# Kernel optimization log

Hardware: AMD Instinct MI355X
Metric: run time of the kernel (lower is better)

The kernel has to match this reference:

```python
import jax, jax.numpy as jnp
import numpy as np

B, T, H, A = 64, 512, 1024, 256  # T == max_sen_len by construction of attention_u
PAD_VAL = -2.0 ** 22


def setup_inputs() -> dict:
    key = jax.random.key(0)
    k1, k2, k3, k4 = jax.random.split(key, 4)
    inputs = jax.random.normal(k1, (B, T, H), dtype=jnp.float32)
    sen_len = jax.random.randint(k2, (B,), 1, T + 1, dtype=jnp.int32)
    W = jax.random.normal(k3, (H, A), dtype=jnp.float32) * (1.0 / np.sqrt(H))
    b = jnp.zeros((A,), dtype=jnp.float32)
    U = jax.random.normal(k4, (A, T), dtype=jnp.float32) * (1.0 / np.sqrt(A))
    return {"inputs": inputs, "sen_len": sen_len, "W": W, "b": b, "U": U}


def reference(inputs, sen_len, W, b, U):
    # Dense with tanh: [B,T,H] @ [H,A] -> [B,T,A]
    alpha = jnp.tanh(jnp.einsum('bth,ha->bta', inputs, W) + b)
    # Score against attention_u: [B,T,A] @ [A,T] -> [B,T,T]
    scores = jnp.einsum('bta,as->bts', alpha, U)
    # sequence mask over last (key) dim, broadcast over query dim
    mask = jnp.arange(T)[None, :] < sen_len[:, None]        # [B,T]
    scores = jnp.where(mask[:, None, :], scores, jnp.float32(PAD_VAL))
    p = jax.nn.softmax(scores, axis=-1)                     # [B,T,T]
    # Weighted sum pooling: [B,T,T] @ [B,T,H] -> [B,T,H]
    Z = jnp.einsum('bts,bsh->bth', p, inputs)
    # dropout: is_training=False -> identity
    return Z
```

## Files before the change

kernel.cpp:

```cpp
#include <hip/hip_runtime.h>
#include <hip/hip_bf16.h>

typedef short short8 __attribute__((ext_vector_type(8)));
typedef short short4v __attribute__((ext_vector_type(4)));
typedef float f32x4 __attribute__((ext_vector_type(4)));
typedef __bf16 bf16x8 __attribute__((ext_vector_type(8)));

template <int ROWS>
__device__ __forceinline__ void stage2(const __hip_bfloat16* __restrict__ g,
                                       int ld, short* lds, int t) {
    const int w = t >> 6;
    const int lane = t & 63;
#pragma unroll
    for (int i = 0; i < ROWS / 64; ++i) {
        const int cb = i * 512 + w * 64;
        const int c = cb + lane;
        const int row = c >> 3;
        const int kc = (c & 7) ^ (row & 7);
        __builtin_amdgcn_global_load_lds((const void*)(g + (long)row * ld + kc * 8),
                                         (void*)(lds + cb * 8), 16, 0, 0);
    }
}

__global__ __launch_bounds__(512, 2) void gemm_xw_kernel(
    const float* __restrict__ Xf,
    const __hip_bfloat16* __restrict__ Wt,
    __hip_bfloat16* __restrict__ alpha,
    const float* __restrict__ bias) {
    __shared__ __align__(16) short sm[2][24576];

    int bx = blockIdx.x, by = blockIdx.y;
    {
        const int nx = gridDim.x, ny = gridDim.y;
        const int nwg = nx * ny;
        const int lin = bx + nx * by;
        const int swz = (lin & 7) * (nwg >> 3) + (lin >> 3);
        bx = swz % nx;
        by = swz / nx;
    }

    const int t = threadIdx.x;
    const int w = t >> 6, lane = t & 63;
    const int wm = w >> 1, wn = w & 1;
    const int fr = lane & 15, quad = lane >> 4;

    const float* Ab = Xf + (long)by * 256 * 1024;
    const __hip_bfloat16* Bb = Wt + (long)bx * 128 * 1024;

    int arow[4], akc[4];
#pragma unroll
    for (int i = 0; i < 4; ++i) {
        const int c = i * 512 + t;
        arow[i] = c >> 3;
        akc[i] = ((c & 7) ^ (arow[i] & 7)) * 8;
    }

    f32x4 acc[4][4] = {};
    float4 rA[4][2];

#pragma unroll
    for (int i = 0; i < 4; ++i) {
        const float* src = Ab + (long)arow[i] * 1024 + akc[i];
        rA[i][0] = *(const float4*)(src);
        rA[i][1] = *(const float4*)(src + 4);
    }
    stage2<128>(Bb, 1024, &sm[0][16384], t);
#pragma unroll
    for (int i = 0; i < 4; ++i) {
        const int c = i * 512 + t;
        __hip_bfloat16 tmp[8] __attribute__((aligned(16)));
        tmp[0] = __float2bfloat16(rA[i][0].x); tmp[1] = __float2bfloat16(rA[i][0].y);
        tmp[2] = __float2bfloat16(rA[i][0].z); tmp[3] = __float2bfloat16(rA[i][0].w);
        tmp[4] = __float2bfloat16(rA[i][1].x); tmp[5] = __float2bfloat16(rA[i][1].y);
        tmp[6] = __float2bfloat16(rA[i][1].z); tmp[7] = __float2bfloat16(rA[i][1].w);
        *(short8*)(void*)&sm[0][c * 8] = *(short8*)(void*)tmp;
    }
    __syncthreads();

    int cur = 0;
    for (int kt = 0; kt < 16; ++kt) {
        const bool more = kt + 1 < 16;
        if (more) {
#pragma unroll
            for (int i = 0; i < 4; ++i) {
                const float* src = Ab + (long)arow[i] * 1024 + (kt + 1) * 64 + akc[i];
                rA[i][0] = *(const float4*)(src);
                rA[i][1] = *(const float4*)(src + 4);
            }
            stage2<128>(Bb + (kt + 1) * 64, 1024, &sm[cur ^ 1][16384], t);
        }
        const short* At = &sm[cur][0];
        const short* Bts = &sm[cur][16384];
#pragma unroll
        for (int ks = 0; ks < 2; ++ks) {
            bf16x8 af[4], bfv[4];
            const int kc = ks * 4 + quad;
#pragma unroll
            for (int m = 0; m < 4; ++m) {
                const int row = wm * 64 + m * 16 + fr;
                const int chunk = row * 8 + (kc ^ (row & 7));
                af[m] = *(const bf16x8*)(const void*)(At + chunk * 8);
            }
#pragma unroll
            for (int n = 0; n < 4; ++n) {
                const int row = wn * 64 + n * 16 + fr;
                const int chunk = row * 8 + (kc ^ (row & 7));
                bfv[n] = *(const bf16x8*)(const void*)(Bts + chunk * 8);
            }
#pragma unroll
            for (int m = 0; m < 4; ++m)
#pragma unroll
                for (int n = 0; n < 4; ++n)
                    acc[m][n] = __builtin_amdgcn_mfma_f32_16x16x32_bf16(
                        af[m], bfv[n], acc[m][n], 0, 0, 0);
        }
        if (more) {
#pragma unroll
            for (int i = 0; i < 4; ++i) {
                const int c = i * 512 + t;
                __hip_bfloat16 tmp[8] __attribute__((aligned(16)));
                tmp[0] = __float2bfloat16(rA[i][0].x); tmp[1] = __float2bfloat16(rA[i][0].y);
                tmp[2] = __float2bfloat16(rA[i][0].z); tmp[3] = __float2bfloat16(rA[i][0].w);
                tmp[4] = __float2bfloat16(rA[i][1].x); tmp[5] = __float2bfloat16(rA[i][1].y);
                tmp[6] = __float2bfloat16(rA[i][1].z); tmp[7] = __float2bfloat16(rA[i][1].w);
                *(short8*)(void*)&sm[cur ^ 1][c * 8] = *(short8*)(void*)tmp;
            }
            __syncthreads();
        }
        cur ^= 1;
    }

    const long rowBase = (long)by * 256 + wm * 64;
    const int colBase = bx * 128 + wn * 64;
#pragma unroll
    for (int m = 0; m < 4; ++m) {
#pragma unroll
        for (int n = 0; n < 4; ++n) {
            const int col = colBase + n * 16 + fr;
            const float bv = bias[col];
#pragma unroll
            for (int j = 0; j < 4; ++j) {
                const long row = rowBase + m * 16 + quad * 4 + j;
                alpha[row * 256 + col] = __float2bfloat16(tanhf(acc[m][n][j] + bv));
            }
        }
    }
}

__global__ __launch_bounds__(512, 4) void gemm_pv_kernel(
    const __hip_bfloat16* __restrict__ P,
    const float* __restrict__ Xf,
    float* __restrict__ Z) {
    __shared__ __align__(16) short smA[2][8192];
    __shared__ __align__(16) short smB[2][5120];

    int bx = blockIdx.x, by = blockIdx.y, bz = blockIdx.z;
    {
        const int nx = gridDim.x, ny = gridDim.y;
        const int nwg = nx * ny * gridDim.z;
        const int lin = bx + nx * (by + ny * bz);
        const int swz = (lin & 7) * (nwg >> 3) + (lin >> 3);
        bx = swz % nx;
        const int r = swz / nx;
        by = r % ny;
        bz = r / ny;
    }

    const int t = threadIdx.x;
    const int w = t >> 6, lane = t & 63;
    const int wm = w >> 1, wn = w & 1;
    const int fr = lane & 15, quad = lane >> 4;

    const __hip_bfloat16* Ab = P + ((long)bz * 512 + by * 256) * 512;
    const float* Bb = Xf + (long)bz * 512 * 1024 + bx * 128;

    int acb[2], arow[2], akc[2];
#pragma unroll
    for (int i = 0; i < 2; ++i) {
        acb[i] = i * 512 + w * 64;
        const int s = acb[i] + lane;
        arow[i] = s >> 2;
        akc[i] = ((s & 3) ^ ((arow[i] >> 1) & 3)) * 8;
    }
    const int bi = t & 15;
    const int bhc = t >> 4;

    f32x4 acc[4][4] = {};
    float4 r0, r1;

#pragma unroll
    for (int i = 0; i < 2; ++i)
        __builtin_amdgcn_global_load_lds(
            (const void*)(Ab + (long)arow[i] * 512 + akc[i]),
            (void*)(&smA[0][acb[i] * 8]), 16, 0, 0);
    {
        const float* s0 = Bb + (long)(2 * bi) * 1024 + bhc * 4;
        r0 = *(const float4*)(s0);
        r1 = *(const float4*)(s0 + 1024);
        int* dst = (int*)(void*)&smB[0][(bhc * 4) * 40 + bi * 2];
#pragma unroll
        for (int j = 0; j < 4; ++j) {
            __hip_bfloat16 h0 = __float2bfloat16(((const float*)&r0)[j]);
            __hip_bfloat16 h1 = __float2bfloat16(((const float*)&r1)[j]);
            dst[j * 20] = (int)*(unsigned short*)&h0 |
                          ((int)*(unsigned short*)&h1 << 16);
        }
    }
    __syncthreads();

    int cur = 0;
    for (int kt = 0; kt < 16; ++kt) {
        const bool more = kt + 1 < 16;
        if (more) {
#pragma unroll
            for (int i = 0; i < 2; ++i)
                __builtin_amdgcn_global_load_lds(
                    (const void*)(Ab + (long)arow[i] * 512 + (kt + 1) * 32 + akc[i]),
                    (void*)(&smA[cur ^ 1][acb[i] * 8]), 16, 0, 0);
            const float* s0 = Bb + (long)((kt + 1) * 32 + 2 * bi) * 1024 + bhc * 4;
            r0 = *(const float4*)(s0);
            r1 = *(const float4*)(s0 + 1024);
        }
        {
            const short* At = &smA[cur][0];
            const short* Bt = &smB[cur][0];
            bf16x8 bfv[4];
#pragma unroll
            for (int n = 0; n < 4; ++n) {
                const int h = wn * 64 + n * 16 + fr;
                bfv[n] = *(const bf16x8*)(const void*)(Bt + h * 40 + quad * 8);
            }
#pragma unroll
            for (int m = 0; m < 4; ++m) {
                const int row = wm * 64 + m * 16 + fr;
                const int slot = row * 4 + (quad ^ ((row >> 1) & 3));
                const bf16x8 af = *(const bf16x8*)(const void*)(At + slot * 8);
#pragma unroll
                for (int n = 0; n < 4; ++n)
                    acc[m][n] = __builtin_amdgcn_mfma_f32_16x16x32_bf16(
                        af, bfv[n], acc[m][n], 0, 0, 0);
            }
        }
        if (more) {
            int* dst = (int*)(void*)&smB[cur ^ 1][(bhc * 4) * 40 + bi * 2];
#pragma unroll
            for (int j = 0; j < 4; ++j) {
                __hip_bfloat16 h0 = __float2bfloat16(((const float*)&r0)[j]);
                __hip_bfloat16 h1 = __float2bfloat16(((const float*)&r1)[j]);
                dst[j * 20] = (int)*(unsigned short*)&h0 |
                              ((int)*(unsigned short*)&h1 << 16);
            }
            __syncthreads();
        }
        cur ^= 1;
    }

    const long rowBase = (long)bz * 512 + by * 256 + wm * 64;
    const int colBase = bx * 128 + wn * 64;
#pragma unroll
    for (int m = 0; m < 4; ++m) {
#pragma unroll
        for (int n = 0; n < 4; ++n) {
            const int col = colBase + n * 16 + fr;
#pragma unroll
            for (int j = 0; j < 4; ++j) {
                const long row = rowBase + m * 16 + quad * 4 + j;
                Z[row * 1024 + col] = acc[m][n][j];
            }
        }
    }
}

__global__ __launch_bounds__(256) void transpose_cvt_kernel(const float* __restrict__ in,
                                                            __hip_bfloat16* __restrict__ out,
                                                            int R, int C) {
    const int o = blockIdx.x * 256 + threadIdx.x;
    if (o >= R * C) return;
    const int c = o / R;
    const int r = o - c * R;
    out[o] = __float2bfloat16(in[(long)r * C + c]);
}

__global__ __launch_bounds__(512) void score_softmax_kernel(
    const __hip_bfloat16* __restrict__ Aa,
    const __hip_bfloat16* __restrict__ Ut,
    __hip_bfloat16* __restrict__ P,
    const int* __restrict__ sen) {
    __shared__ __align__(16) short At[64 * 64];
    __shared__ __align__(16) short Bts[512 * 64];
    __shared__ float red[2][64][9];

    const int t = threadIdx.x;
    const int w = t >> 6, lane = t & 63;
    const int fr = lane & 15, quad = lane >> 4;
    const long row0 = (long)blockIdx.x * 64;
    const __hip_bfloat16* Ab = Aa + row0 * 256;

    f32x4 acc[4][4] = {};

    for (int kt = 0; kt < 4; ++kt) {
        if (kt) __syncthreads();
        {
            const int cb = w * 64;
            const int c = cb + lane;
            const int row = c >> 3, kc = (c & 7) ^ (row & 7);
            __builtin_amdgcn_global_load_lds(
                (const void*)(Ab + (long)row * 256 + kt * 64 + kc * 8),
                (void*)(At + cb * 8), 16, 0, 0);
        }
#pragma unroll
        for (int i = 0; i < 8; ++i) {
            const int cb = i * 512 + w * 64;
            const int c = cb + lane;
            const int row = c >> 3, kc = (c & 7) ^ (row & 7);
            __builtin_amdgcn_global_load_lds(
                (const void*)(Ut + (long)row * 256 + kt * 64 + kc * 8),
                (void*)(Bts + cb * 8), 16, 0, 0);
        }
        __syncthreads();
#pragma unroll
        for (int ks = 0; ks < 2; ++ks) {
            bf16x8 af[4], bfv[4];
            const int kc = ks * 4 + quad;
#pragma unroll
            for (int m = 0; m < 4; ++m) {
                const int row = m * 16 + fr;
                const int chunk = row * 8 + (kc ^ (row & 7));
                af[m] = *(const bf16x8*)(const void*)(At + chunk * 8);
            }
#pragma unroll
            for (int n = 0; n < 4; ++n) {
                const int row = w * 64 + n * 16 + fr;
                const int chunk = row * 8 + (kc ^ (row & 7));
                bfv[n] = *(const bf16x8*)(const void*)(Bts + chunk * 8);
            }
#pragma unroll
            for (int m = 0; m < 4; ++m)
#pragma unroll
                for (int n = 0; n < 4; ++n)
                    acc[m][n] = __builtin_amdgcn_mfma_f32_16x16x32_bf16(
                        af[m], bfv[n], acc[m][n], 0, 0, 0);
        }
    }
    __syncthreads();

    const int L = sen[row0 >> 9];
    bool valid[4];
#pragma unroll
    for (int n = 0; n < 4; ++n) valid[n] = (w * 64 + n * 16 + fr) < L;

    float mx[4][4];
#pragma unroll
    for (int m = 0; m < 4; ++m)
#pragma unroll
        for (int j = 0; j < 4; ++j) {
            float v = -3.0e38f;
#pragma unroll
            for (int n = 0; n < 4; ++n)
                if (valid[n]) v = fmaxf(v, acc[m][n][j]);
#pragma unroll
            for (int off = 8; off >= 1; off >>= 1) v = fmaxf(v, __shfl_xor(v, off, 64));
            mx[m][j] = v;
        }
    if (fr == 0) {
#pragma unroll
        for (int m = 0; m < 4; ++m)
#pragma unroll
            for (int j = 0; j < 4; ++j) red[0][m * 16 + quad * 4 + j][w] = mx[m][j];
    }
    __syncthreads();
    float rmax[4][4];
#pragma unroll
    for (int m = 0; m < 4; ++m)
#pragma unroll
        for (int j = 0; j < 4; ++j) {
            const int row = m * 16 + quad * 4 + j;
            float v = red[0][row][0];
#pragma unroll
            for (int ww = 1; ww < 8; ++ww) v = fmaxf(v, red[0][row][ww]);
            rmax[m][j] = v;
        }

    float sum[4][4];
#pragma unroll
    for (int m = 0; m < 4; ++m)
#pragma unroll
        for (int j = 0; j < 4; ++j) {
            float s = 0.f;
#pragma unroll
            for (int n = 0; n < 4; ++n) {
                float e = valid[n] ? __expf(acc[m][n][j] - rmax[m][j]) : 0.f;
                acc[m][n][j] = e;
                s += e;
            }
#pragma unroll
            for (int off = 8; off >= 1; off >>= 1) s += __shfl_xor(s, off, 64);
            sum[m][j] = s;
        }
    if (fr == 0) {
#pragma unroll
        for (int m = 0; m < 4; ++m)
#pragma unroll
            for (int j = 0; j < 4; ++j) red[1][m * 16 + quad * 4 + j][w] = sum[m][j];
    }
    __syncthreads();
#pragma unroll
    for (int m = 0; m < 4; ++m)
#pragma unroll
        for (int j = 0; j < 4; ++j) {
            const int row = m * 16 + quad * 4 + j;
            float s = 0.f;
#pragma unroll
            for (int ww = 0; ww < 8; ++ww) s += red[1][row][ww];
            const float inv = 1.f / s;
#pragma unroll
            for (int n = 0; n < 4; ++n)
                P[(row0 + row) * 512 + w * 64 + n * 16 + fr] =
                    __float2bfloat16(acc[m][n][j] * inv);
        }
}

extern "C" void kernel_launch(void* const* d_in, const int* in_sizes, int n_in,
                              void* d_out, int out_size, void* d_ws, size_t ws_size,
                              hipStream_t stream) {
    const float* X = (const float*)d_in[0];
    const int* sen = (const int*)d_in[1];
    const float* W = (const float*)d_in[2];
    const float* bias = (const float*)d_in[3];
    const float* U = (const float*)d_in[4];
    float* out = (float*)d_out;

    const int B = 64, T = 512, H = 1024, A = 256;
    const long M = (long)B * T;

    char* ws = (char*)d_ws;
    __hip_bfloat16* Pbf = (__hip_bfloat16*)ws;
    __hip_bfloat16* Wt = (__hip_bfloat16*)(ws + M * T * 2);
    __hip_bfloat16* Ut = (__hip_bfloat16*)((char*)Wt + (long)H * A * 2);

    __hip_bfloat16* alpha = (__hip_bfloat16*)((char*)d_out + M * H * 2);

    transpose_cvt_kernel<<<(H * A) / 256, 256, 0, stream>>>(W, Wt, H, A);
    transpose_cvt_kernel<<<(A * T) / 256, 256, 0, stream>>>(U, Ut, A, T);
    gemm_xw_kernel<<<dim3(2, 128), 512, 0, stream>>>(X, Wt, alpha, bias);
    score_softmax_kernel<<<(int)(M / 64), 512, 0, stream>>>(alpha, Ut, Pbf, sen);
    gemm_pv_kernel<<<dim3(H / 128, T / 256, B), 512, 0, stream>>>(Pbf, X, out);
}
```

Baseline: 157.8 us.

## Triple-buffer P tiles in PV GEMM with explicit waitcnt pipelining

```diff
diff --git a/kernel.cpp b/kernel.cpp
--- a/kernel.cpp
+++ b/kernel.cpp
@@ -151,7 +151,7 @@
     const __hip_bfloat16* __restrict__ P,
     const float* __restrict__ Xf,
     float* __restrict__ Z) {
-    __shared__ __align__(16) short smA[2][8192];
+    __shared__ __align__(16) short smA[3][8192];
     __shared__ __align__(16) short smB[2][5120];
 
     int bx = blockIdx.x, by = blockIdx.y, bz = blockIdx.z;
@@ -188,42 +188,47 @@
     f32x4 acc[4][4] = {};
     float4 r0, r1;
 
-#pragma unroll
-    for (int i = 0; i < 2; ++i)
-        __builtin_amdgcn_global_load_lds(
-            (const void*)(Ab + (long)arow[i] * 512 + akc[i]),
-            (void*)(&smA[0][acb[i] * 8]), 16, 0, 0);
-    {
-        const float* s0 = Bb + (long)(2 * bi) * 1024 + bhc * 4;
-        r0 = *(const float4*)(s0);
-        r1 = *(const float4*)(s0 + 1024);
-        int* dst = (int*)(void*)&smB[0][(bhc * 4) * 40 + bi * 2];
-#pragma unroll
-        for (int j = 0; j < 4; ++j) {
-            __hip_bfloat16 h0 = __float2bfloat16(((const float*)&r0)[j]);
-            __hip_bfloat16 h1 = __float2bfloat16(((const float*)&r1)[j]);
-            dst[j * 20] = (int)*(unsigned short*)&h0 |
-                          ((int)*(unsigned short*)&h1 << 16);
-        }
-    }
-    __syncthreads();
-
-    int cur = 0;
-    for (int kt = 0; kt < 16; ++kt) {
-        const bool more = kt + 1 < 16;
-        if (more) {
-#pragma unroll
-            for (int i = 0; i < 2; ++i)
-                __builtin_amdgcn_global_load_lds(
-                    (const void*)(Ab + (long)arow[i] * 512 + (kt + 1) * 32 + akc[i]),
-                    (void*)(&smA[cur ^ 1][acb[i] * 8]), 16, 0, 0);
-            const float* s0 = Bb + (long)((kt + 1) * 32 + 2 * bi) * 1024 + bhc * 4;
-            r0 = *(const float4*)(s0);
-            r1 = *(const float4*)(s0 + 1024);
-        }
+#define PV_ISSUE_A(KT, BUF)                                                     \
+    _Pragma("unroll") for (int i = 0; i < 2; ++i)                               \
+        __builtin_amdgcn_global_load_lds(                                       \
+            (const void*)(Ab + (long)arow[i] * 512 + (KT) * 32 + akc[i]),       \
+            (void*)(&smA[BUF][acb[i] * 8]), 16, 0, 0);
+
+#define PV_LOAD_B(KT)                                                           \
+    {                                                                           \
+        const float* s0 = Bb + (long)((KT) * 32 + 2 * bi) * 1024 + bhc * 4;     \
+        r0 = *(const float4*)(s0);                                              \
+        r1 = *(const float4*)(s0 + 1024);                                       \
+    }
+
+#define PV_WRITE_B(BUF)                                                         \
+    {                                                                           \
+        int* dst = (int*)(void*)&smB[BUF][(bhc * 4) * 40 + bi * 2];             \
+        _Pragma("unroll") for (int j = 0; j < 4; ++j) {                         \
+            __hip_bfloat16 h0 = __float2bfloat16(((const float*)&r0)[j]);       \
+            __hip_bfloat16 h1 = __float2bfloat16(((const float*)&r1)[j]);       \
+            dst[j * 20] = (int)*(unsigned short*)&h0 |                          \
+                          ((int)*(unsigned short*)&h1 << 16);                   \
+        }                                                                       \
+    }
+
+    PV_ISSUE_A(0, 0)
+    PV_ISSUE_A(1, 1)
+    PV_LOAD_B(0)
+    PV_WRITE_B(0)
+    PV_LOAD_B(1)
+    __builtin_amdgcn_sched_barrier(0);
+    asm volatile("s_waitcnt vmcnt(4)" ::: "memory");
+    asm volatile("s_waitcnt lgkmcnt(0)" ::: "memory");
+    __builtin_amdgcn_s_barrier();
+    __builtin_amdgcn_sched_barrier(0);
+
+#pragma unroll
+    for (int k = 0; k < 16; ++k) {
+        if (k + 2 < 16) PV_ISSUE_A(k + 2, (k + 2) % 3)
         {
-            const short* At = &smA[cur][0];
-            const short* Bt = &smB[cur][0];
+            const short* At = &smA[k % 3][0];
+            const short* Bt = &smB[k % 2][0];
             bf16x8 bfv[4];
 #pragma unroll
             for (int n = 0; n < 4; ++n) {
@@ -241,19 +246,23 @@
                         af, bfv[n], acc[m][n], 0, 0, 0);
             }
         }
-        if (more) {
-            int* dst = (int*)(void*)&smB[cur ^ 1][(bhc * 4) * 40 + bi * 2];
-#pragma unroll
-            for (int j = 0; j < 4; ++j) {
-                __hip_bfloat16 h0 = __float2bfloat16(((const float*)&r0)[j]);
-                __hip_bfloat16 h1 = __float2bfloat16(((const float*)&r1)[j]);
-                dst[j * 20] = (int)*(unsigned short*)&h0 |
-                              ((int)*(unsigned short*)&h1 << 16);
-            }
-            __syncthreads();
-        }
-        cur ^= 1;
-    }
+        if (k + 1 < 16) PV_WRITE_B((k + 1) % 2)
+        if (k + 2 < 16) PV_LOAD_B(k + 2)
+        __builtin_amdgcn_sched_barrier(0);
+        if (k + 2 < 16) {
+            asm volatile("s_waitcnt vmcnt(4)" ::: "memory");
+        } else if (k + 1 < 16) {
+            asm volatile("s_waitcnt vmcnt(0)" ::: "memory");
+        }
+        if (k + 1 < 16) {
+            asm volatile("s_waitcnt lgkmcnt(0)" ::: "memory");
+            __builtin_amdgcn_s_barrier();
+            __builtin_amdgcn_sched_barrier(0);
+        }
+    }
+#undef PV_ISSUE_A
+#undef PV_LOAD_B
+#undef PV_WRITE_B
 
     const long rowBase = (long)bz * 512 + by * 256 + wm * 64;
     const int colBase = bx * 128 + wn * 64;
```

After: 144.1 us. 8.7% less time.
